# Performance work log

Measured on AMD Instinct MI355X. Metric: run time of the kernel, lower is better.

## Reference

```python
import jax, jax.numpy as jnp
import numpy as np

D_MODEL, N_STATE, L_MAX, BATCH = 256, 64, 2048, 16

def _to_c(x):
    return jax.lax.complex(x[..., 0], x[..., 1])

def setup_inputs() -> dict:
    key = jax.random.key(0)
    k_u, k_ct_r, k_ct_i, k_step = jax.random.split(key, 4)
    n, d = N_STATE, D_MODEL
    # --- HiPPO DPLR init (numpy, matches torch hippo_dplr) ---
    P = np.sqrt(1.0 + 2.0 * np.arange(1, n + 1, dtype=np.float64))
    A = np.tril(np.outer(P, P)) - np.diag(np.arange(1, n + 1, dtype=np.float64))
    A = -A
    p = 0.5 * np.sqrt(2.0 * np.arange(1, n + 1, dtype=np.float64) + 1.0)
    Ap = (A + np.outer(p, p)).astype(np.complex64)
    lam, V = np.linalg.eig(Ap)
    p_rot = V.conj().T @ p.astype(np.complex64)
    p_ri = np.stack([p_rot.real, p_rot.imag], -1).astype(np.float32)          # (n,2)
    lambda_ri = np.stack([lam.real, lam.imag], -1).astype(np.float32)         # (n,2)
    # --- B init: sqrt(2k+1), repeated over channels, zero imag ---
    B_r = np.sqrt(2.0 * np.arange(1, n + 1) + 1.0).astype(np.float32)
    B_ri = np.stack([np.tile(B_r, (d, 1)), np.zeros((d, n), np.float32)], -1) # (d,n,2)
    # --- Ct: xavier-normal complex ---
    std = float(np.sqrt(2.0 / (d + n)))
    Ct_r = jax.random.normal(k_ct_r, (d, n), jnp.float32) * (std / np.sqrt(2.0))
    Ct_i = jax.random.normal(k_ct_i, (d, n), jnp.float32) * (std / np.sqrt(2.0))
    Ct_ri = jnp.stack([Ct_r, Ct_i], -1)                                        # (d,n,2)
    Dp = jnp.ones((1, 1, d), jnp.float32)
    log_step = jax.random.uniform(k_step, (d,), jnp.float32) * (
        np.log(0.1) - np.log(0.001)) + np.log(0.001)
    u = jax.random.normal(k_u, (BATCH, L_MAX, d), jnp.float32)
    return {"u": u, "p_ri": jnp.asarray(p_ri), "lambda_ri": jnp.asarray(lambda_ri),
            "B_ri": jnp.asarray(B_ri), "Ct_ri": Ct_ri, "Dp": Dp, "log_step": log_step}

def reference(u, p_ri, lambda_ri, B_ri, Ct_ri, Dp, log_step):
    p = _to_c(p_ri)          # (n,)
    lam = _to_c(lambda_ri)   # (n,)
    B = _to_c(B_ri)          # (d,n)
    Ct = _to_c(Ct_ri)        # (d,n)
    L = u.shape[1]
    omega = jnp.exp(2j * jnp.pi * jnp.arange(L) / L).astype(jnp.complex64)  # (L,)
    step = jnp.exp(log_step)                                               # (d,)
    g = (2.0 / step)[:, None] * ((1.0 - omega) / (1.0 + omega))[None, :]   # (d,L)
    c = 2.0 / (1.0 + omega)                                                # (L,)
    inv = 1.0 / (g[:, :, None] - lam[None, None, :])                       # (d,L,n)
    k00 = jnp.einsum('dn,dln->dl', Ct.conj() * B, inv)
    k01 = jnp.einsum('dn,dln->dl', Ct.conj() * p[None, :], inv)
    k10 = jnp.einsum('dn,dln->dl', p.conj()[None, :] * B, inv)
    k11 = jnp.einsum('n,dln->dl', p.conj() * p, inv)
    at_roots = c[None, :] * (k00 - k01 * k10 / (1.0 + k11))                # (d,L)
    out = jnp.fft.ifft(at_roots, n=L, axis=-1)
    order = jnp.concatenate([jnp.zeros((1,), jnp.int32), jnp.arange(L - 1, 0, -1)])
    K = out[:, order].real[None]                                           # (1,d,L)
    # causal FFT convolution
    ud = jnp.fft.rfft(jnp.pad(u, ((0, 0), (0, L), (0, 0))), axis=1)        # (B,L+1,d)
    Kd = jnp.fft.rfft(jnp.pad(K, ((0, 0), (0, 0), (0, L))), axis=-1)       # (1,d,L+1)
    y = jnp.fft.irfft(jnp.transpose(ud, (0, 2, 1)) * Kd, axis=-1)[..., :L]
    y = jnp.transpose(y, (0, 2, 1)).astype(u.dtype)                        # (B,L,d)
    return y + Dp * u
```

## Files before the change

### kernel.cpp

```cpp
#include <hip/hip_runtime.h>
#include <math.h>

#define LLEN   2048
#define NFFT   4096
#define DMODEL 256
#define NSTATE 64
#define NBATCH 16
#define PI_F   3.14159265358979323846f

#define PADIDX(a) ((a) + ((a) >> 4))
#define LDSN2 (LLEN + (LLEN >> 4))
#define KSTRIDE 2056

#define SWZIDX(a) ((a) ^ (((a) >> 4) & 15))

__device__ inline float frcp(float x) { return __builtin_amdgcn_rcpf(x); }

#define RADIX4(ar0,ai0,ar1,ai1,ar2,ai2,ar3,ai3,S) do {                      \
    float s0r=(ar0)+(ar2), s0i=(ai0)+(ai2);                                 \
    float s1r=(ar0)-(ar2), s1i=(ai0)-(ai2);                                 \
    float s2r=(ar1)+(ar3), s2i=(ai1)+(ai3);                                 \
    float s3r=(ar1)-(ar3), s3i=(ai1)-(ai3);                                 \
    (ar0)=s0r+s2r; (ai0)=s0i+s2i;                                           \
    (ar2)=s0r-s2r; (ai2)=s0i-s2i;                                           \
    (ar1)=s1r-(S)*s3i; (ai1)=s1i+(S)*s3r;                                   \
    (ar3)=s1r+(S)*s3i; (ai3)=s1i-(S)*s3r;                                   \
} while (0)

template<int SIGN>
__device__ inline void dft16(float xr[16], float xi[16]) {
    const float S = (float)SIGN;
    const float C1 = 0.9238795325112867f, S1 = 0.3826834323650898f;
    const float C2 = 0.7071067811865476f;
    RADIX4(xr[0],xi[0], xr[4],xi[4], xr[8],xi[8],  xr[12],xi[12], S);
    RADIX4(xr[1],xi[1], xr[5],xi[5], xr[9],xi[9],  xr[13],xi[13], S);
    RADIX4(xr[2],xi[2], xr[6],xi[6], xr[10],xi[10],xr[14],xi[14], S);
    RADIX4(xr[3],xi[3], xr[7],xi[7], xr[11],xi[11],xr[15],xi[15], S);
#define TW(idx, wr_, wi_) { float tr = xr[idx]*(wr_) - xi[idx]*(wi_);       \
    xi[idx] = xr[idx]*(wi_) + xi[idx]*(wr_); xr[idx] = tr; }
    TW(5,  C1,  S*S1);
    TW(6,  C2,  S*C2);
    TW(7,  S1,  S*C1);
    TW(9,  C2,  S*C2);
    TW(10, 0.f, S);
    TW(11, -C2, S*C2);
    TW(13, S1,  S*C1);
    TW(14, -C2, S*C2);
    TW(15, -C1, -S*S1);
#undef TW
    RADIX4(xr[0],xi[0],  xr[1],xi[1],  xr[2],xi[2],  xr[3],xi[3],  S);
    RADIX4(xr[4],xi[4],  xr[5],xi[5],  xr[6],xi[6],  xr[7],xi[7],  S);
    RADIX4(xr[8],xi[8],  xr[9],xi[9],  xr[10],xi[10],xr[11],xi[11],S);
    RADIX4(xr[12],xi[12],xr[13],xi[13],xr[14],xi[14],xr[15],xi[15],S);
}

template<int SIGN>
__device__ inline void dft8(float xr[8], float xi[8]) {
    const float S = (float)SIGN;
    const float C2 = 0.7071067811865476f;
    RADIX4(xr[0],xi[0], xr[2],xi[2], xr[4],xi[4], xr[6],xi[6], S);
    RADIX4(xr[1],xi[1], xr[3],xi[3], xr[5],xi[5], xr[7],xi[7], S);
    { float tr = xr[3]*C2 - xi[3]*(S*C2); xi[3] = xr[3]*(S*C2) + xi[3]*C2; xr[3] = tr; }
    { float tr = -S*xi[5]; xi[5] = S*xr[5]; xr[5] = tr; }
    { float tr = xr[7]*(-C2) - xi[7]*(S*C2); xi[7] = xr[7]*(S*C2) + xi[7]*(-C2); xr[7] = tr; }
    float br[8], bi[8];
#pragma unroll
    for (int k = 0; k < 4; ++k) {
        br[k]   = xr[2*k] + xr[2*k+1]; bi[k]   = xi[2*k] + xi[2*k+1];
        br[k+4] = xr[2*k] - xr[2*k+1]; bi[k+4] = xi[2*k] - xi[2*k+1];
    }
#pragma unroll
    for (int k = 0; k < 8; ++k) { xr[k] = br[k]; xi[k] = bi[k]; }
}

template<int SIGN>
__device__ inline void tw_apply16(float xr[16], float xi[16], float ang) {
    float wr[16], wi[16];
    __sincosf(ang, &wi[1], &wr[1]);
#pragma unroll
    for (int k = 1; k < 8; ++k) {
        wr[2*k]   = wr[k]*wr[k] - wi[k]*wi[k];
        wi[2*k]   = 2.f * wr[k] * wi[k];
        wr[2*k+1] = wr[k]*wr[k+1] - wi[k]*wi[k+1];
        wi[2*k+1] = wr[k]*wi[k+1] + wi[k]*wr[k+1];
    }
#pragma unroll
    for (int t = 1; t < 16; ++t) {
        float tr = xr[t]*wr[t] - xi[t]*wi[t];
        xi[t] = xr[t]*wi[t] + xi[t]*wr[t];
        xr[t] = tr;
    }
}

template<int SIGN, int M, int L, bool PRUNE>
__device__ inline void stage16(float2* X, int j, bool active) {
    float xr[16], xi[16];
    const int p = j & (L - 1);
    if (active) {
#pragma unroll
        for (int t = 0; t < 16; ++t) {
            float2 v = X[PADIDX(j + t * M)];
            xr[t] = v.x; xi[t] = v.y;
        }
        tw_apply16<SIGN>(xr, xi, ((float)SIGN * 2.f * PI_F / (float)(16 * L)) * (float)p);
        dft16<SIGN>(xr, xi);
    }
    __syncthreads();
    if (active) {
        const int base = 16 * j - 15 * p;
#pragma unroll
        for (int k0 = 0; k0 < 4; ++k0)
#pragma unroll
            for (int k2 = 0; k2 < 4; ++k2) {
                const int u = k0 + 4 * k2;
                if (!PRUNE || u < 8) {
                    const int a = base + u * L;
                    X[PADIDX(a)] = make_float2(xr[4*k0+k2], xi[4*k0+k2]);
                }
            }
    }
    __syncthreads();
}

template<int SIGN>
__device__ inline void fft2048_f2(float2* X, int tid) {
    float xr[8], xi[8];
#pragma unroll
    for (int t = 0; t < 8; ++t) {
        float2 v = X[PADIDX(tid + t * 256)];
        xr[t] = v.x; xi[t] = v.y;
    }
    dft8<SIGN>(xr, xi);
    __syncthreads();
#pragma unroll
    for (int u = 0; u < 8; ++u)
        X[PADIDX(8 * tid + u)] = make_float2(xr[u], xi[u]);
    __syncthreads();
    stage16<SIGN, 128, 8,   false>(X, tid, tid < 128);
    stage16<SIGN, 128, 128, false>(X, tid, tid < 128);
}

template<int SIGN, int M, int L, bool PRUNE>
__device__ inline void stage16s(float2* X, int j) {
    float xr[16], xi[16];
    const int p = j & (L - 1);
#pragma unroll
    for (int t = 0; t < 16; ++t) {
        float2 v = X[SWZIDX(j + t * M)];
        xr[t] = v.x; xi[t] = v.y;
    }
    tw_apply16<SIGN>(xr, xi, ((float)SIGN * 2.f * PI_F / (float)(16 * L)) * (float)p);
    dft16<SIGN>(xr, xi);
    __syncthreads();
    const int base = 16 * j - 15 * p;
#pragma unroll
    for (int k0 = 0; k0 < 4; ++k0)
#pragma unroll
        for (int k2 = 0; k2 < 4; ++k2) {
            const int u = k0 + 4 * k2;
            if (!PRUNE || u < 8) {
                const int a = base + u * L;
                X[SWZIDX(a)] = make_float2(xr[4*k0+k2], xi[4*k0+k2]);
            }
        }
    __syncthreads();
}

template<int SIGN, bool PRUNE>
__device__ inline void fft4096_swz_from_regs(float2* X, int tid,
                                             float xr[16], float xi[16]) {
    dft16<SIGN>(xr, xi);
#pragma unroll
    for (int k0 = 0; k0 < 4; ++k0)
#pragma unroll
        for (int k2 = 0; k2 < 4; ++k2)
            X[SWZIDX(16 * tid + k0 + 4 * k2)] = make_float2(xr[4*k0+k2], xi[4*k0+k2]);
    __syncthreads();
    stage16s<SIGN, 256, 16,  false>(X, tid);
    stage16s<SIGN, 256, 256, PRUNE>(X, tid);
}

template<int SIGN, bool PRUNE>
__device__ inline void fft4096_swz(float2* X, int tid) {
    float xr[16], xi[16];
#pragma unroll
    for (int t = 0; t < 16; ++t) {
        float2 v = X[SWZIDX(tid + t * 256)];
        xr[t] = v.x; xi[t] = v.y;
    }
    dft16<SIGN>(xr, xi);
    __syncthreads();
#pragma unroll
    for (int k0 = 0; k0 < 4; ++k0)
#pragma unroll
        for (int k2 = 0; k2 < 4; ++k2)
            X[SWZIDX(16 * tid + k0 + 4 * k2)] = make_float2(xr[4*k0+k2], xi[4*k0+k2]);
    __syncthreads();
    stage16s<SIGN, 256, 16,  false>(X, tid);
    stage16s<SIGN, 256, 256, PRUNE>(X, tid);
}

__global__ __launch_bounds__(256) void k_ar(const float* __restrict__ p_ri,
                                            const float* __restrict__ lambda_ri,
                                            const float* __restrict__ B_ri,
                                            const float* __restrict__ Ct_ri,
                                            const float* __restrict__ log_step,
                                            float2* __restrict__ ar_out) {
    __shared__ float4 c0[NSTATE], c1[NSTATE];
    __shared__ float2 lam[NSTATE];
    const int d = blockIdx.x >> 1;
    const int lbase = (blockIdx.x & 1) << 10;
    const int tid = threadIdx.x;
    if (tid < NSTATE) {
        const int n = tid;
        const float px = p_ri[2*n], py = p_ri[2*n+1];
        lam[n] = make_float2(lambda_ri[2*n], lambda_ri[2*n+1]);
        const float Bx = B_ri[(d*NSTATE+n)*2], By = B_ri[(d*NSTATE+n)*2+1];
        const float Cx = Ct_ri[(d*NSTATE+n)*2], Cy = Ct_ri[(d*NSTATE+n)*2+1];
        c0[n] = make_float4(Cx*Bx + Cy*By, Cx*By - Cy*Bx,
                            Cx*px + Cy*py, Cx*py - Cy*px);
        c1[n] = make_float4(px*Bx + py*By, px*By - py*Bx, px*px + py*py, 0.f);
    }
    __syncthreads();

    const float tos = 2.f * __expf(-log_step[d]);
    float gx[4], gy[4], ccx[4], ccy[4];
    float k00x[4], k00y[4], k01x[4], k01y[4];
    float k10x[4], k10y[4], k11x[4], k11y[4];
#pragma unroll
    for (int j = 0; j < 4; ++j) {
        const int l = lbase + tid + (j << 8);
        float sn, cs;
        sincosf(2.f * PI_F * (float)l / (float)LLEN, &sn, &cs);
        const float opx = 1.f + cs, opy = sn;
        const float omx = 1.f - cs, omy = -sn;
        const float inv_op = frcp(opx*opx + opy*opy);
        gx[j] = tos * (omx*opx + omy*opy) * inv_op;
        gy[j] = tos * (omy*opx - omx*opy) * inv_op;
        ccx[j] = 2.f * opx * inv_op; ccy[j] = -2.f * opy * inv_op;
        k00x[j]=0.f; k00y[j]=0.f; k01x[j]=0.f; k01y[j]=0.f;
        k10x[j]=0.f; k10y[j]=0.f; k11x[j]=0.f; k11y[j]=0.f;
    }
    for (int n = 0; n < NSTATE; ++n) {
        const float2 lm = lam[n];
        const float4 a = c0[n];
        const float4 b = c1[n];
#pragma unroll
        for (int j = 0; j < 4; ++j) {
            const float dx = gx[j] - lm.x, dy = gy[j] - lm.y;
            const float idn = frcp(dx*dx + dy*dy);
            const float ix = dx * idn, iy = -dy * idn;
            k00x[j] += a.x*ix - a.y*iy;  k00y[j] += a.x*iy + a.y*ix;
            k01x[j] += a.z*ix - a.w*iy;  k01y[j] += a.z*iy + a.w*ix;
            k10x[j] += b.x*ix - b.y*iy;  k10y[j] += b.x*iy + b.y*ix;
            k11x[j] += b.z*ix;           k11y[j] += b.z*iy;
        }
    }
#pragma unroll
    for (int j = 0; j < 4; ++j) {
        const float nx = k01x[j]*k10x[j] - k01y[j]*k10y[j];
        const float ny = k01x[j]*k10y[j] + k01y[j]*k10x[j];
        const float dpx = 1.f + k11x[j], dpy = k11y[j];
        const float idq = frcp(dpx*dpx + dpy*dpy);
        const float qx = (nx*dpx + ny*dpy) * idq;
        const float qy = (ny*dpx - nx*dpy) * idq;
        const float rx = k00x[j] - qx, ry = k00y[j] - qy;
        ar_out[(size_t)d * LLEN + lbase + tid + (j << 8)] =
            make_float2(ccx[j]*rx - ccy[j]*ry, ccx[j]*ry + ccy[j]*rx);
    }
}

__global__ __launch_bounds__(256, 4) void k_mix(const float* __restrict__ u,
                                                const float2* __restrict__ a_in,
                                                float* __restrict__ ut,
                                                float2* __restrict__ Hc) {
    __shared__ float2 X[LDSN2];
    const int tid = threadIdx.x;

    if (blockIdx.x >= DMODEL) {
        const int blk = blockIdx.x - DMODEL;
        const int bt0 = (blk & 511) * 64;
        const int ch0 = (blk >> 9) * 64;
        float* tile = (float*)X;
        const int tx4 = (tid & 15) * 4;
        const int ty  = tid >> 4;
#pragma unroll
        for (int k = 0; k < 4; ++k) {
            const int r = ty + 16 * k;
            const float4 v = *(const float4*)&u[(size_t)(bt0 + r) * DMODEL + ch0 + tx4];
            tile[r * 65 + tx4 + 0] = v.x;
            tile[r * 65 + tx4 + 1] = v.y;
            tile[r * 65 + tx4 + 2] = v.z;
            tile[r * 65 + tx4 + 3] = v.w;
        }
        __syncthreads();
#pragma unroll
        for (int k = 0; k < 4; ++k) {
            const int c = ty + 16 * k;
            float4 o;
            o.x = tile[(tx4 + 0) * 65 + c];
            o.y = tile[(tx4 + 1) * 65 + c];
            o.z = tile[(tx4 + 2) * 65 + c];
            o.w = tile[(tx4 + 3) * 65 + c];
            *(float4*)&ut[(size_t)(ch0 + c) * (NBATCH * LLEN) + bt0 + tx4] = o;
        }
        return;
    }

    const int d = blockIdx.x;
    const float isc = 1.f / (float)NFFT;
    const float4* a4 = (const float4*)(a_in + (size_t)d * LLEN);
#pragma unroll
    for (int k = 0; k < 4; ++k) {
        const int v = tid + k * 256;
        const float4 w = a4[v];
        X[PADIDX(2 * v)]     = make_float2(w.x, w.y);
        X[PADIDX(2 * v + 1)] = make_float2(w.z, w.w);
    }
    __syncthreads();

    float2* H = Hc + (size_t)d * KSTRIDE;
    for (int m = tid; m <= 1024; m += 256) {
        const float2 am = X[PADIDX(m)];
        const float2 an = X[PADIDX((LLEN - m) & (LLEN - 1))];
        H[2 * m] = make_float2((an.x + am.x) * 0.5f * isc,
                               (an.y - am.y) * 0.5f * isc);
    }
    fft2048_f2<-1>(X, tid);

#pragma unroll
    for (int k = 0; k < 8; ++k) {
        const int j = tid + k * 256;
        const int q = PADIDX(j);
        const float Kj = X[q].x * (1.f / (float)LLEN);
        float snj, csj;
        __sincosf(-PI_F * (float)j * (1.f / 2048.f), &snj, &csj);
        X[q] = make_float2(Kj * csj, Kj * snj);
    }
    __syncthreads();
    fft2048_f2<-1>(X, tid);

    for (int m = tid; m < 1024; m += 256) {
        const float2 w = X[PADIDX(m)];
        H[2 * m + 1] = make_float2(w.x * isc, w.y * isc);
    }
}

__global__ __launch_bounds__(256, 4) void k_conv(const float* __restrict__ ut,
                                                 const float2* __restrict__ Hc,
                                                 const float* __restrict__ Dp,
                                                 float* __restrict__ yt) {
    __shared__ float2 X[NFFT];
    const int bid = blockIdx.x;
    const int x = bid & 7;
    const int s = bid >> 3;
    const int ch = (x << 5) | (s & 31);
    const int pair = s >> 5;
    const int tid = threadIdx.x;

    const float* u0 = ut + (size_t)ch * (NBATCH * LLEN) + (size_t)(2 * pair) * LLEN;
    const float* u1 = u0 + LLEN;

    float xr[16], xi[16];
#pragma unroll
    for (int k = 0; k < 8; ++k) {
        xr[k] = u0[tid + k * 256];
        xi[k] = u1[tid + k * 256];
    }
#pragma unroll
    for (int k = 8; k < 16; ++k) { xr[k] = 0.f; xi[k] = 0.f; }

    fft4096_swz_from_regs<-1, false>(X, tid, xr, xi);

    const float2* H = Hc + (size_t)ch * KSTRIDE;
    for (int f = tid; f <= NFFT / 2; f += 256) {
        const int fb = (NFFT - f) & (NFFT - 1);
        const float2 Za = X[SWZIDX(f)], Zb = X[SWZIDX(fb)];
        const float u0x = 0.5f * (Za.x + Zb.x), u0y = 0.5f * (Za.y - Zb.y);
        const float u1x = 0.5f * (Za.y + Zb.y), u1y = -0.5f * (Za.x - Zb.x);
        const float2 Ha = H[f];
        const float y0x = u0x*Ha.x - u0y*Ha.y, y0y = u0x*Ha.y + u0y*Ha.x;
        const float y1x = u1x*Ha.x - u1y*Ha.y, y1y = u1x*Ha.y + u1y*Ha.x;
        X[SWZIDX(f)] = make_float2(y0x - y1y, y0y + y1x);
        if (fb != f) {
            const float Hbx = Ha.x, Hby = -Ha.y;
            const float z0x = u0x*Hbx + u0y*Hby, z0y = u0x*Hby - u0y*Hbx;
            const float z1x = u1x*Hbx + u1y*Hby, z1y = u1x*Hby - u1y*Hbx;
            X[SWZIDX(fb)] = make_float2(z0x - z1y, z0y + z1x);
        }
    }
    __syncthreads();
    fft4096_swz<+1, true>(X, tid);

    const float dp = Dp[ch];
    float* y0o = yt + (size_t)ch * (NBATCH * LLEN) + (size_t)(2 * pair) * LLEN;
    float* y1o = y0o + LLEN;
#pragma unroll
    for (int k = 0; k < 2; ++k) {
        const int i0 = 4 * (tid + k * 256);
        const float2 va = X[SWZIDX(i0 + 0)];
        const float2 vb = X[SWZIDX(i0 + 1)];
        const float2 vc = X[SWZIDX(i0 + 2)];
        const float2 vd = X[SWZIDX(i0 + 3)];
        const float4 u0v = *(const float4*)&u0[i0];
        const float4 u1v = *(const float4*)&u1[i0];
        float4 o0, o1;
        o0.x = va.x + dp * u0v.x; o0.y = vb.x + dp * u0v.y;
        o0.z = vc.x + dp * u0v.z; o0.w = vd.x + dp * u0v.w;
        o1.x = va.y + dp * u1v.x; o1.y = vb.y + dp * u1v.y;
        o1.z = vc.y + dp * u1v.z; o1.w = vd.y + dp * u1v.w;
        *(float4*)&y0o[i0] = o0;
        *(float4*)&y1o[i0] = o1;
    }
}

__global__ __launch_bounds__(256) void k_post(const float* __restrict__ yt,
                                              float* __restrict__ out) {
    __shared__ float tile[64 * 65];
    const int bt0 = (blockIdx.x & 511) * 64;
    const int ch0 = (blockIdx.x >> 9) * 64;
    const int tid = threadIdx.x;
    const int tx4 = (tid & 15) * 4;
    const int ty  = tid >> 4;
#pragma unroll
    for (int k = 0; k < 4; ++k) {
        const int r = ty + 16 * k;
        const float4 v = *(const float4*)&yt[(size_t)(ch0 + r) * (NBATCH * LLEN) + bt0 + tx4];
        tile[r * 65 + tx4 + 0] = v.x;
        tile[r * 65 + tx4 + 1] = v.y;
        tile[r * 65 + tx4 + 2] = v.z;
        tile[r * 65 + tx4 + 3] = v.w;
    }
    __syncthreads();
#pragma unroll
    for (int k = 0; k < 4; ++k) {
        const int b = ty + 16 * k;
        float4 o;
        o.x = tile[(tx4 + 0) * 65 + b];
        o.y = tile[(tx4 + 1) * 65 + b];
        o.z = tile[(tx4 + 2) * 65 + b];
        o.w = tile[(tx4 + 3) * 65 + b];
        *(float4*)&out[(size_t)(bt0 + b) * DMODEL + ch0 + tx4] = o;
    }
}

extern "C" void kernel_launch(void* const* d_in, const int* in_sizes, int n_in,
                              void* d_out, int out_size, void* d_ws, size_t ws_size,
                              hipStream_t stream) {
    const float* u         = (const float*)d_in[0];
    const float* p_ri      = (const float*)d_in[1];
    const float* lambda_ri = (const float*)d_in[2];
    const float* B_ri      = (const float*)d_in[3];
    const float* Ct_ri     = (const float*)d_in[4];
    const float* Dp        = (const float*)d_in[5];
    const float* log_step  = (const float*)d_in[6];
    float* out = (float*)d_out;

    float2* Hc = (float2*)d_ws;
    char*   wb = (char*)d_ws + (size_t)DMODEL * KSTRIDE * sizeof(float2);
    float2* a  = (float2*)wb;
    float*  yt = (float*)wb;
    float*  ut = out;

    k_ar  <<<DMODEL * 2, 256, 0, stream>>>(p_ri, lambda_ri, B_ri, Ct_ri, log_step, a);
    k_mix <<<DMODEL + 2048, 256, 0, stream>>>(u, a, ut, Hc);
    k_conv<<<DMODEL * (NBATCH / 2), 256, 0, stream>>>(ut, Hc, Dp, yt);
    k_post<<<2048, 256, 0, stream>>>(yt, out);
}
```

Baseline: 170.8 us.

## Fuse Cauchy-kernel evaluation into k_mix and prune zero-padded first FFT stage

Merges the k_ar kernel into k_mix, so each channel block computes its 2048 at-roots values directly into shared memory instead of writing them to global memory and reading them back. This removes one kernel launch and the global round trip. The cost is 256 heavier blocks doing all 2048 points serially, which lowers parallelism for the Cauchy sum. It also adds a dft16z variant that skips the zero upper half of the padded input in the conv FFT's first radix-4 stage, saving some arithmetic and register initialisation.

Result: no change. 173.4 us (+1.5%).

```diff
diff --git a/kernel.cpp b/kernel.cpp
--- a/kernel.cpp
+++ b/kernel.cpp
@@ -28,14 +28,10 @@
 } while (0)
 
 template<int SIGN>
-__device__ inline void dft16(float xr[16], float xi[16]) {
+__device__ inline void dft16_tail(float xr[16], float xi[16]) {
     const float S = (float)SIGN;
     const float C1 = 0.9238795325112867f, S1 = 0.3826834323650898f;
     const float C2 = 0.7071067811865476f;
-    RADIX4(xr[0],xi[0], xr[4],xi[4], xr[8],xi[8],  xr[12],xi[12], S);
-    RADIX4(xr[1],xi[1], xr[5],xi[5], xr[9],xi[9],  xr[13],xi[13], S);
-    RADIX4(xr[2],xi[2], xr[6],xi[6], xr[10],xi[10],xr[14],xi[14], S);
-    RADIX4(xr[3],xi[3], xr[7],xi[7], xr[11],xi[11],xr[15],xi[15], S);
 #define TW(idx, wr_, wi_) { float tr = xr[idx]*(wr_) - xi[idx]*(wi_);       \
     xi[idx] = xr[idx]*(wi_) + xi[idx]*(wr_); xr[idx] = tr; }
     TW(5,  C1,  S*S1);
@@ -55,6 +51,34 @@
 }
 
 template<int SIGN>
+__device__ inline void dft16(float xr[16], float xi[16]) {
+    const float S = (float)SIGN;
+    RADIX4(xr[0],xi[0], xr[4],xi[4], xr[8],xi[8],  xr[12],xi[12], S);
+    RADIX4(xr[1],xi[1], xr[5],xi[5], xr[9],xi[9],  xr[13],xi[13], S);
+    RADIX4(xr[2],xi[2], xr[6],xi[6], xr[10],xi[10],xr[14],xi[14], S);
+    RADIX4(xr[3],xi[3], xr[7],xi[7], xr[11],xi[11],xr[15],xi[15], S);
+    dft16_tail<SIGN>(xr, xi);
+}
+
+template<int SIGN>
+__device__ inline void dft16z(float xr[16], float xi[16]) {
+    const float S = (float)SIGN;
+#define RAD4Z(r0,i0,r1,i1,r2,i2,r3,i3) do {                                 \
+    const float a0r=(r0), a0i=(i0), a1r=(r1), a1i=(i1);                     \
+    (r0)=a0r+a1r;     (i0)=a0i+a1i;                                         \
+    (r2)=a0r-a1r;     (i2)=a0i-a1i;                                         \
+    (r1)=a0r-S*a1i;   (i1)=a0i+S*a1r;                                       \
+    (r3)=a0r+S*a1i;   (i3)=a0i-S*a1r;                                       \
+} while (0)
+    RAD4Z(xr[0],xi[0], xr[4],xi[4], xr[8],xi[8],  xr[12],xi[12]);
+    RAD4Z(xr[1],xi[1], xr[5],xi[5], xr[9],xi[9],  xr[13],xi[13]);
+    RAD4Z(xr[2],xi[2], xr[6],xi[6], xr[10],xi[10],xr[14],xi[14]);
+    RAD4Z(xr[3],xi[3], xr[7],xi[7], xr[11],xi[11],xr[15],xi[15]);
+#undef RAD4Z
+    dft16_tail<SIGN>(xr, xi);
+}
+
+template<int SIGN>
 __device__ inline void dft8(float xr[8], float xi[8]) {
     const float S = (float)SIGN;
     const float C2 = 0.7071067811865476f;
@@ -169,7 +193,7 @@
 template<int SIGN, bool PRUNE>
 __device__ inline void fft4096_swz_from_regs(float2* X, int tid,
                                              float xr[16], float xi[16]) {
-    dft16<SIGN>(xr, xi);
+    dft16z<SIGN>(xr, xi);
 #pragma unroll
     for (int k0 = 0; k0 < 4; ++k0)
 #pragma unroll
@@ -200,17 +224,51 @@
     stage16s<SIGN, 256, 256, PRUNE>(X, tid);
 }
 
-__global__ __launch_bounds__(256) void k_ar(const float* __restrict__ p_ri,
-                                            const float* __restrict__ lambda_ri,
-                                            const float* __restrict__ B_ri,
-                                            const float* __restrict__ Ct_ri,
-                                            const float* __restrict__ log_step,
-                                            float2* __restrict__ ar_out) {
+__global__ __launch_bounds__(256, 4) void k_mix(const float* __restrict__ u,
+                                                const float* __restrict__ p_ri,
+                                                const float* __restrict__ lambda_ri,
+                                                const float* __restrict__ B_ri,
+                                                const float* __restrict__ Ct_ri,
+                                                const float* __restrict__ log_step,
+                                                float* __restrict__ ut,
+                                                float2* __restrict__ Hc) {
+    __shared__ float2 X[LDSN2];
     __shared__ float4 c0[NSTATE], c1[NSTATE];
     __shared__ float2 lam[NSTATE];
-    const int d = blockIdx.x >> 1;
-    const int lbase = (blockIdx.x & 1) << 10;
     const int tid = threadIdx.x;
+
+    if (blockIdx.x >= DMODEL) {
+        const int blk = blockIdx.x - DMODEL;
+        const int bt0 = (blk & 511) * 64;
+        const int ch0 = (blk >> 9) * 64;
+        float* tile = (float*)X;
+        const int tx4 = (tid & 15) * 4;
+        const int ty  = tid >> 4;
+#pragma unroll
+        for (int k = 0; k < 4; ++k) {
+            const int r = ty + 16 * k;
+            const float4 v = *(const float4*)&u[(size_t)(bt0 + r) * DMODEL + ch0 + tx4];
+            tile[r * 65 + tx4 + 0] = v.x;
+            tile[r * 65 + tx4 + 1] = v.y;
+            tile[r * 65 + tx4 + 2] = v.z;
+            tile[r * 65 + tx4 + 3] = v.w;
+        }
+        __syncthreads();
+#pragma unroll
+        for (int k = 0; k < 4; ++k) {
+            const int c = ty + 16 * k;
+            float4 o;
+            o.x = tile[(tx4 + 0) * 65 + c];
+            o.y = tile[(tx4 + 1) * 65 + c];
+            o.z = tile[(tx4 + 2) * 65 + c];
+            o.w = tile[(tx4 + 3) * 65 + c];
+            *(float4*)&ut[(size_t)(ch0 + c) * (NBATCH * LLEN) + bt0 + tx4] = o;
+        }
+        return;
+    }
+
+    const int d = blockIdx.x;
+
     if (tid < NSTATE) {
         const int n = tid;
         const float px = p_ri[2*n], py = p_ri[2*n+1];
@@ -224,101 +282,58 @@
     __syncthreads();
 
     const float tos = 2.f * __expf(-log_step[d]);
-    float gx[4], gy[4], ccx[4], ccy[4];
-    float k00x[4], k00y[4], k01x[4], k01y[4];
-    float k10x[4], k10y[4], k11x[4], k11y[4];
-#pragma unroll
-    for (int j = 0; j < 4; ++j) {
-        const int l = lbase + tid + (j << 8);
-        float sn, cs;
-        sincosf(2.f * PI_F * (float)l / (float)LLEN, &sn, &cs);
-        const float opx = 1.f + cs, opy = sn;
-        const float omx = 1.f - cs, omy = -sn;
-        const float inv_op = frcp(opx*opx + opy*opy);
-        gx[j] = tos * (omx*opx + omy*opy) * inv_op;
-        gy[j] = tos * (omy*opx - omx*opy) * inv_op;
-        ccx[j] = 2.f * opx * inv_op; ccy[j] = -2.f * opy * inv_op;
-        k00x[j]=0.f; k00y[j]=0.f; k01x[j]=0.f; k01y[j]=0.f;
-        k10x[j]=0.f; k10y[j]=0.f; k11x[j]=0.f; k11y[j]=0.f;
-    }
-    for (int n = 0; n < NSTATE; ++n) {
-        const float2 lm = lam[n];
-        const float4 a = c0[n];
-        const float4 b = c1[n];
+#pragma unroll
+    for (int chunk = 0; chunk < 2; ++chunk) {
+        const int lbase = chunk << 10;
+        float gx[4], gy[4], ccx[4], ccy[4];
+        float k00x[4], k00y[4], k01x[4], k01y[4];
+        float k10x[4], k10y[4], k11x[4], k11y[4];
 #pragma unroll
         for (int j = 0; j < 4; ++j) {
-            const float dx = gx[j] - lm.x, dy = gy[j] - lm.y;
-            const float idn = frcp(dx*dx + dy*dy);
-            const float ix = dx * idn, iy = -dy * idn;
-            k00x[j] += a.x*ix - a.y*iy;  k00y[j] += a.x*iy + a.y*ix;
-            k01x[j] += a.z*ix - a.w*iy;  k01y[j] += a.z*iy + a.w*ix;
-            k10x[j] += b.x*ix - b.y*iy;  k10y[j] += b.x*iy + b.y*ix;
-            k11x[j] += b.z*ix;           k11y[j] += b.z*iy;
-        }
-    }
-#pragma unroll
-    for (int j = 0; j < 4; ++j) {
-        const float nx = k01x[j]*k10x[j] - k01y[j]*k10y[j];
-        const float ny = k01x[j]*k10y[j] + k01y[j]*k10x[j];
-        const float dpx = 1.f + k11x[j], dpy = k11y[j];
-        const float idq = frcp(dpx*dpx + dpy*dpy);
-        const float qx = (nx*dpx + ny*dpy) * idq;
-        const float qy = (ny*dpx - nx*dpy) * idq;
-        const float rx = k00x[j] - qx, ry = k00y[j] - qy;
-        ar_out[(size_t)d * LLEN + lbase + tid + (j << 8)] =
-            make_float2(ccx[j]*rx - ccy[j]*ry, ccx[j]*ry + ccy[j]*rx);
-    }
-}
-
-__global__ __launch_bounds__(256, 4) void k_mix(const float* __restrict__ u,
-                                                const float2* __restrict__ a_in,
-                                                float* __restrict__ ut,
-                                                float2* __restrict__ Hc) {
-    __shared__ float2 X[LDSN2];
-    const int tid = threadIdx.x;
-
-    if (blockIdx.x >= DMODEL) {
-        const int blk = blockIdx.x - DMODEL;
-        const int bt0 = (blk & 511) * 64;
-        const int ch0 = (blk >> 9) * 64;
-        float* tile = (float*)X;
-        const int tx4 = (tid & 15) * 4;
-        const int ty  = tid >> 4;
-#pragma unroll
-        for (int k = 0; k < 4; ++k) {
-            const int r = ty + 16 * k;
-            const float4 v = *(const float4*)&u[(size_t)(bt0 + r) * DMODEL + ch0 + tx4];
-            tile[r * 65 + tx4 + 0] = v.x;
-            tile[r * 65 + tx4 + 1] = v.y;
-            tile[r * 65 + tx4 + 2] = v.z;
-            tile[r * 65 + tx4 + 3] = v.w;
-        }
-        __syncthreads();
-#pragma unroll
-        for (int k = 0; k < 4; ++k) {
-            const int c = ty + 16 * k;
-            float4 o;
-            o.x = tile[(tx4 + 0) * 65 + c];
-            o.y = tile[(tx4 + 1) * 65 + c];
-            o.z = tile[(tx4 + 2) * 65 + c];
-            o.w = tile[(tx4 + 3) * 65 + c];
-            *(float4*)&ut[(size_t)(ch0 + c) * (NBATCH * LLEN) + bt0 + tx4] = o;
-        }
-        return;
-    }
-
-    const int d = blockIdx.x;
+            const int l = lbase + tid + (j << 8);
+            float sn, cs;
+            sincosf(2.f * PI_F * (float)l / (float)LLEN, &sn, &cs);
+            const float opx = 1.f + cs, opy = sn;
+            const float omx = 1.f - cs, omy = -sn;
+            const float inv_op = frcp(opx*opx + opy*opy);
+            gx[j] = tos * (omx*opx + omy*opy) * inv_op;
+            gy[j] = tos * (omy*opx - omx*opy) * inv_op;
+            ccx[j] = 2.f * opx * inv_op; ccy[j] = -2.f * opy * inv_op;
+            k00x[j]=0.f; k00y[j]=0.f; k01x[j]=0.f; k01y[j]=0.f;
+            k10x[j]=0.f; k10y[j]=0.f; k11x[j]=0.f; k11y[j]=0.f;
+        }
+        for (int n = 0; n < NSTATE; ++n) {
+            const float2 lm = lam[n];
+            const float4 a = c0[n];
+            const float4 b = c1[n];
+#pragma unroll
+            for (int j = 0; j < 4; ++j) {
+                const float dx = gx[j] - lm.x, dy = gy[j] - lm.y;
+                const float idn = frcp(dx*dx + dy*dy);
+                const float ix = dx * idn, iy = -dy * idn;
+                k00x[j] += a.x*ix - a.y*iy;  k00y[j] += a.x*iy + a.y*ix;
+                k01x[j] += a.z*ix - a.w*iy;  k01y[j] += a.z*iy + a.w*ix;
+                k10x[j] += b.x*ix - b.y*iy;  k10y[j] += b.x*iy + b.y*ix;
+                k11x[j] += b.z*ix;           k11y[j] += b.z*iy;
+            }
+        }
+#pragma unroll
+        for (int j = 0; j < 4; ++j) {
+            const float nx = k01x[j]*k10x[j] - k01y[j]*k10y[j];
+            const float ny = k01x[j]*k10y[j] + k01y[j]*k10x[j];
+            const float dpx = 1.f + k11x[j], dpy = k11y[j];
+            const float idq = frcp(dpx*dpx + dpy*dpy);
+            const float qx = (nx*dpx + ny*dpy) * idq;
+            const float qy = (ny*dpx - nx*dpy) * idq;
+            const float rx = k00x[j] - qx, ry = k00y[j] - qy;
+            const int l = lbase + tid + (j << 8);
+            X[PADIDX(l)] = make_float2(ccx[j]*rx - ccy[j]*ry,
+                                       ccx[j]*ry + ccy[j]*rx);
+        }
+    }
+    __syncthreads();
+
     const float isc = 1.f / (float)NFFT;
-    const float4* a4 = (const float4*)(a_in + (size_t)d * LLEN);
-#pragma unroll
-    for (int k = 0; k < 4; ++k) {
-        const int v = tid + k * 256;
-        const float4 w = a4[v];
-        X[PADIDX(2 * v)]     = make_float2(w.x, w.y);
-        X[PADIDX(2 * v + 1)] = make_float2(w.z, w.w);
-    }
-    __syncthreads();
-
     float2* H = Hc + (size_t)d * KSTRIDE;
     for (int m = tid; m <= 1024; m += 256) {
         const float2 am = X[PADIDX(m)];
@@ -367,8 +382,6 @@
         xr[k] = u0[tid + k * 256];
         xi[k] = u1[tid + k * 256];
     }
-#pragma unroll
-    for (int k = 8; k < 16; ++k) { xr[k] = 0.f; xi[k] = 0.f; }
 
     fft4096_swz_from_regs<-1, false>(X, tid, xr, xi);
 
@@ -457,13 +470,11 @@
     float* out = (float*)d_out;
 
     float2* Hc = (float2*)d_ws;
-    char*   wb = (char*)d_ws + (size_t)DMODEL * KSTRIDE * sizeof(float2);
-    float2* a  = (float2*)wb;
-    float*  yt = (float*)wb;
+    float*  yt = (float*)((char*)d_ws + (size_t)DMODEL * KSTRIDE * sizeof(float2));
     float*  ut = out;
 
-    k_ar  <<<DMODEL * 2, 256, 0, stream>>>(p_ri, lambda_ri, B_ri, Ct_ri, log_step, a);
-    k_mix <<<DMODEL + 2048, 256, 0, stream>>>(u, a, ut, Hc);
+    k_mix <<<DMODEL + 2048, 256, 0, stream>>>(u, p_ri, lambda_ri, B_ri, Ct_ri,
+                                              log_step, ut, Hc);
     k_conv<<<DMODEL * (NBATCH / 2), 256, 0, stream>>>(ut, Hc, Dp, yt);
     k_post<<<2048, 256, 0, stream>>>(yt, out);
 }
```
